# Kernel optimization log

Measured on AMD Instinct MI355X. Metric: run time of the kernel, lower is better.

The kernel has to match this reference:

```python
import jax, jax.numpy as jnp
import numpy as np

N_NODES = 10000
N_EDGES = 80000
F_IN = 128
H1 = 2048
H2 = 2048
H3 = 1024


def _sgconv(x, pos, src, dst, W_in, b_in, W_out, b_out):
    # geo-GCN SpatialGraphConv with hidden_size=1:
    # message(j->i) = relu(Linear(pos_j - pos_i)) * x_j ; aggr='add' ; then Linear out
    rel = pos[src] - pos[dst]                      # [E, 2]  (pos_j - pos_i)
    scale = jax.nn.relu(rel @ W_in + b_in)         # [E, C_in]
    msg = scale * x[src]                           # [E, C_in]
    agg = jax.ops.segment_sum(msg, dst, num_segments=x.shape[0])  # [N, C_in]
    return agg @ W_out + b_out                     # [N, C_out]


def setup_inputs() -> dict:
    key = jax.random.key(0)
    ks = jax.random.split(key, 12)
    x = jax.random.normal(ks[0], (N_NODES, F_IN), dtype=jnp.float32)
    pos = jax.random.normal(ks[1], (N_NODES, 2), dtype=jnp.float32)
    edge_index = jax.random.randint(ks[2], (2, N_EDGES), 0, N_NODES, dtype=jnp.int32)

    def lin(k, fan_in, fan_out):
        lim = 1.0 / np.sqrt(fan_in)
        kw, kb = jax.random.split(k)
        W = jax.random.uniform(kw, (fan_in, fan_out), jnp.float32, -lim, lim)
        b = jax.random.uniform(kb, (fan_out,), jnp.float32, -lim, lim)
        return W, b

    W_in1, b_in1 = lin(ks[3], 2, F_IN)
    W_out1, b_out1 = lin(ks[4], F_IN, H1)
    W_in2, b_in2 = lin(ks[5], 2, H1)
    W_out2, b_out2 = lin(ks[6], H1, H2)
    W_in3, b_in3 = lin(ks[7], 2, H2)
    W_out3, b_out3 = lin(ks[8], H2, H3)

    return {
        "x": x, "pos": pos, "edge_index": edge_index,
        "W_in1": W_in1, "b_in1": b_in1, "W_out1": W_out1, "b_out1": b_out1,
        "W_in2": W_in2, "b_in2": b_in2, "W_out2": W_out2, "b_out2": b_out2,
        "W_in3": W_in3, "b_in3": b_in3, "W_out3": W_out3, "b_out3": b_out3,
    }


def reference(x, pos, edge_index,
              W_in1, b_in1, W_out1, b_out1,
              W_in2, b_in2, W_out2, b_out2,
              W_in3, b_in3, W_out3, b_out3):
    src, dst = edge_index[0], edge_index[1]  # flow source_to_target: j=src, i=dst
    h = jax.nn.relu(_sgconv(x, pos, src, dst, W_in1, b_in1, W_out1, b_out1))
    h = jax.nn.relu(_sgconv(h, pos, src, dst, W_in2, b_in2, W_out2, b_out2))
    h = jax.nn.relu(_sgconv(h, pos, src, dst, W_in3, b_in3, W_out3, b_out3))
    # F.normalize(h, dim=1): L2 normalize rows with eps clamp 1e-12
    norm = jnp.linalg.norm(h, axis=1, keepdims=True)
    return h / jnp.maximum(norm, 1e-12)
```

## Files before the change

### kernel.cpp

```cpp
#include <hip/hip_runtime.h>
#include <hip/hip_bf16.h>

#define DEVI __device__ __forceinline__

constexpr int NN = 10000;
constexpr int NE = 80000;
constexpr int AGG_ROWS = 10240;
constexpr int ES_CAP = 110016;

typedef __attribute__((ext_vector_type(8))) short bf16x8;
typedef __attribute__((ext_vector_type(4))) float f32x4;

DEVI float blo(unsigned int u) {
  union { unsigned int i; float f; } c; c.i = u << 16; return c.f;
}
DEVI float bhi(unsigned int u) {
  union { unsigned int i; float f; } c; c.i = u & 0xffff0000u; return c.f;
}
DEVI unsigned short f2b(float f) {
  union { float f; unsigned int i; } c; c.f = f;
  unsigned int i = c.i;
  return (unsigned short)((i + 0x7fffu + ((i >> 16) & 1u)) >> 16);
}
DEVI void st1(float* p, float v) { *p = v; }
DEVI void st1(unsigned short* p, float v) { *p = f2b(v); }
DEVI void store8b(unsigned short* p, const float v[8]) {
  int4 pk;
  pk.x = (int)((unsigned)f2b(v[0]) | ((unsigned)f2b(v[1]) << 16));
  pk.y = (int)((unsigned)f2b(v[2]) | ((unsigned)f2b(v[3]) << 16));
  pk.z = (int)((unsigned)f2b(v[4]) | ((unsigned)f2b(v[5]) << 16));
  pk.w = (int)((unsigned)f2b(v[6]) | ((unsigned)f2b(v[7]) << 16));
  *reinterpret_cast<int4*>(p) = pk;
}

DEVI void gload16(const void* g, void* l) {
  __builtin_amdgcn_global_load_lds(
      (const __attribute__((address_space(1))) void*)g,
      (__attribute__((address_space(3))) void*)l, 16, 0, 0);
}

__global__ __launch_bounds__(256)
void hist_kernel(const int* __restrict__ dst, int* __restrict__ cnt) {
  int e = blockIdx.x * 256 + threadIdx.x;
  if (e < NE) atomicAdd(&cnt[dst[e]], 1);
}

__global__ __launch_bounds__(1024)
void scan_kernel(const int* __restrict__ cnt, int* __restrict__ off,
                 int* __restrict__ cursor) {
  __shared__ int wpart[16];
  __shared__ int carry;
  int tid = threadIdx.x, lane = tid & 63, w = tid >> 6;
  if (tid == 0) carry = 0;
  __syncthreads();
  for (int base = 0; base < NN; base += 1024) {
    int i = base + tid;
    int v = (i < NN) ? ((cnt[i] + 3) & ~3) : 0;
    int s = v;
#pragma unroll
    for (int o = 1; o < 64; o <<= 1) { int t = __shfl_up(s, o); if (lane >= o) s += t; }
    if (lane == 63) wpart[w] = s;
    __syncthreads();
    if (w == 0) {
      int ws = (lane < 16) ? wpart[lane] : 0;
#pragma unroll
      for (int o = 1; o < 16; o <<= 1) { int t = __shfl_up(ws, o); if (lane >= o) ws += t; }
      if (lane < 16) wpart[lane] = ws;
    }
    __syncthreads();
    int ex = carry + (w ? wpart[w - 1] : 0) + s - v;
    if (i < NN) { off[i] = ex; cursor[i] = ex; }
    __syncthreads();
    if (tid == 0) carry += wpart[15];
    __syncthreads();
  }
}

__global__ __launch_bounds__(256)
void bucket_kernel(const int* __restrict__ src, const int* __restrict__ dst,
                   const float* __restrict__ pos,
                   int* __restrict__ cursor, int* __restrict__ es,
                   float* __restrict__ rel) {
  int e = blockIdx.x * 256 + threadIdx.x;
  if (e < NE) {
    int s = src[e], d = dst[e];
    int p = atomicAdd(&cursor[d], 1);
    float2 ps = *reinterpret_cast<const float2*>(pos + 2 * s);
    float2 pd = *reinterpret_cast<const float2*>(pos + 2 * d);
    es[p] = s;
    *reinterpret_cast<float2*>(rel + 2 * p) = make_float2(ps.x - pd.x, ps.y - pd.y);
  }
}

__global__ __launch_bounds__(256)
void transpose_w(const float* __restrict__ W, unsigned short* __restrict__ WT,
                 int K, int N) {
  __shared__ float tile[32][33];
  int tx = threadIdx.x & 31, ty = threadIdx.x >> 5;
  int n0 = blockIdx.x * 32, k0 = blockIdx.y * 32;
#pragma unroll
  for (int j = 0; j < 32; j += 8)
    tile[ty + j][tx] = W[(size_t)(k0 + ty + j) * N + n0 + tx];
  __syncthreads();
#pragma unroll
  for (int j = 0; j < 32; j += 8)
    WT[(size_t)(n0 + ty + j) * K + k0 + tx] = f2b(tile[tx][ty + j]);
}

__global__ __launch_bounds__(256)
void gather_l1(const float* __restrict__ x,
               const int* __restrict__ off, const int* __restrict__ cnt,
               const int* __restrict__ es, const float* __restrict__ rel,
               const float* __restrict__ Win, const float* __restrict__ bin,
               unsigned short* __restrict__ agg) {
  constexpr int C = 128;
  int lane = threadIdx.x & 63;
  int i = blockIdx.x * 4 + (threadIdx.x >> 6);
  if (i >= NN) return;
  int c = lane * 2;
  float w00 = Win[c], w01 = Win[c + 1];
  float w10 = Win[C + c], w11 = Win[C + c + 1];
  float b0 = bin[c], b1 = bin[c + 1];
  float a0 = 0.f, a1 = 0.f;
  int s0 = off[i], n = cnt[i];

  for (int k = 0; k < n; k += 4) {
    int4 s4 = *reinterpret_cast<const int4*>(es + s0 + k);
    float4 ra = *reinterpret_cast<const float4*>(rel + 2 * (s0 + k));
    float4 rb = *reinterpret_cast<const float4*>(rel + 2 * (s0 + k) + 4);
    float2 q0 = *reinterpret_cast<const float2*>(x + (size_t)s4.x * C + c);
    float2 q1 = *reinterpret_cast<const float2*>(x + (size_t)s4.y * C + c);
    float2 q2 = *reinterpret_cast<const float2*>(x + (size_t)s4.z * C + c);
    float2 q3 = *reinterpret_cast<const float2*>(x + (size_t)s4.w * C + c);
    {
      float sc0 = fmaxf(fmaf(ra.x, w00, fmaf(ra.y, w10, b0)), 0.f);
      float sc1 = fmaxf(fmaf(ra.x, w01, fmaf(ra.y, w11, b1)), 0.f);
      a0 = fmaf(sc0, q0.x, a0); a1 = fmaf(sc1, q0.y, a1);
    }
    if (k + 1 < n) {
      float sc0 = fmaxf(fmaf(ra.z, w00, fmaf(ra.w, w10, b0)), 0.f);
      float sc1 = fmaxf(fmaf(ra.z, w01, fmaf(ra.w, w11, b1)), 0.f);
      a0 = fmaf(sc0, q1.x, a0); a1 = fmaf(sc1, q1.y, a1);
    }
    if (k + 2 < n) {
      float sc0 = fmaxf(fmaf(rb.x, w00, fmaf(rb.y, w10, b0)), 0.f);
      float sc1 = fmaxf(fmaf(rb.x, w01, fmaf(rb.y, w11, b1)), 0.f);
      a0 = fmaf(sc0, q2.x, a0); a1 = fmaf(sc1, q2.y, a1);
    }
    if (k + 3 < n) {
      float sc0 = fmaxf(fmaf(rb.z, w00, fmaf(rb.w, w10, b0)), 0.f);
      float sc1 = fmaxf(fmaf(rb.z, w01, fmaf(rb.w, w11, b1)), 0.f);
      a0 = fmaf(sc0, q3.x, a0); a1 = fmaf(sc1, q3.y, a1);
    }
  }
  unsigned int pk = (unsigned)f2b(a0) | ((unsigned)f2b(a1) << 16);
  *reinterpret_cast<unsigned int*>(agg + (size_t)i * C + c) = pk;
}

__global__ __launch_bounds__(256)
void gather_chunk(const unsigned short* __restrict__ x,
                  const int* __restrict__ off, const int* __restrict__ cnt,
                  const int* __restrict__ es, const float* __restrict__ rel,
                  const float* __restrict__ Win, const float* __restrict__ bin,
                  unsigned short* __restrict__ agg, int ngb8) {
  constexpr int C = 2048;
  constexpr int V = 8;
  int wgid = blockIdx.x;
  int half = wgid >= ngb8;
  int base = half ? wgid - ngb8 : wgid;
  int chunk = (base & 7) + (half << 3);
  int grp = base >> 3;
  int lane = threadIdx.x & 63;
  int wid = threadIdx.x >> 6;
  int slot = lane >> 4;
  int l16 = lane & 15;
  int i = grp * 16 + wid * 4 + slot;
  int c = chunk * 128 + l16 * V;

  float w0[V], w1[V], bb[V], acc[V];
#pragma unroll
  for (int j = 0; j < V; ++j) {
    w0[j] = Win[c + j]; w1[j] = Win[C + c + j]; bb[j] = bin[c + j]; acc[j] = 0.f;
  }
  int s0 = off[i], n = cnt[i];

  auto fma8 = [&](float rx, float ry, const int4& q) {
    float xv[V] = { blo(q.x), bhi(q.x), blo(q.y), bhi(q.y),
                    blo(q.z), bhi(q.z), blo(q.w), bhi(q.w) };
#pragma unroll
    for (int j = 0; j < V; ++j) {
      float sc = fmaxf(fmaf(rx, w0[j], fmaf(ry, w1[j], bb[j])), 0.f);
      acc[j] = fmaf(sc, xv[j], acc[j]);
    }
  };
  for (int k = 0; k < n; k += 4) {
    int4 s4 = *reinterpret_cast<const int4*>(es + s0 + k);
    float4 ra = *reinterpret_cast<const float4*>(rel + 2 * (s0 + k));
    float4 rb = *reinterpret_cast<const float4*>(rel + 2 * (s0 + k) + 4);
    int4 q0 = *reinterpret_cast<const int4*>(x + (size_t)s4.x * C + c);
    int4 q1 = *reinterpret_cast<const int4*>(x + (size_t)s4.y * C + c);
    int4 q2 = *reinterpret_cast<const int4*>(x + (size_t)s4.z * C + c);
    int4 q3 = *reinterpret_cast<const int4*>(x + (size_t)s4.w * C + c);
    fma8(ra.x, ra.y, q0);
    if (k + 1 < n) fma8(ra.z, ra.w, q1);
    if (k + 2 < n) fma8(rb.x, rb.y, q2);
    if (k + 3 < n) fma8(rb.z, rb.w, q3);
  }
  store8b(agg + (size_t)i * C + c, acc);
}

template <typename OT>
__global__ __launch_bounds__(512, 2)
void gemm8p(const unsigned short* __restrict__ A,
            const unsigned short* __restrict__ BT,
            const float* __restrict__ bias, OT* __restrict__ out,
            int M, int N, int K) {
  extern __shared__ unsigned short lds[];
  const int t = threadIdx.x;
  const int lane = t & 63, wid = t >> 6;
  const int wr = wid >> 2, wc = wid & 3;

  const int nwg = gridDim.x * gridDim.y;
  const int orig = blockIdx.y * gridDim.x + blockIdx.x;
  const int swz = (orig & 7) * (nwg >> 3) + (orig >> 3);
  const int bx = swz % gridDim.x, by = swz / gridDim.x;
  const int m0 = by * 320, n0 = bx * 256;
  const int nk = K >> 6;

  const int srow = t >> 3;
  const int schunk = (t & 7) ^ (srow & 7);
  const unsigned short* gA = A + (size_t)(m0 + srow) * K + schunk * 8;
  const unsigned short* gB = BT + (size_t)(n0 + srow) * K + schunk * 8;
  const int lt8 = t * 8;

  auto STAGE = [&](int buf, int kt) {
    const size_t ko = (size_t)kt << 6;
    unsigned short* lb = lds + buf * 36864;
#pragma unroll
    for (int jj = 0; jj < 5; ++jj)
      gload16(gA + (size_t)(jj * 64) * K + ko, lb + jj * 4096 + lt8);
#pragma unroll
    for (int jj = 0; jj < 4; ++jj)
      gload16(gB + (size_t)(jj * 64) * K + ko, lb + 20480 + jj * 4096 + lt8);
  };

  const int frow = lane & 15, kc = lane >> 4;
  const int sl0 = (kc ^ (frow & 7)) * 8;
  const int paRow = (wr * 160 + frow) * 64;
  const int pbRow = 20480 + (wc * 64 + frow) * 64;

  f32x4 acc[10][4];
#pragma unroll
  for (int m = 0; m < 10; ++m)
#pragma unroll
    for (int n = 0; n < 4; ++n) acc[m][n] = 0.f;

  STAGE(0, 0);

  int cur = 0;
  for (int kt = 0; kt < nk; ++kt) {
    if (kt + 1 < nk) {
      STAGE(cur ^ 1, kt + 1);
      asm volatile("s_waitcnt vmcnt(9)" ::: "memory");
    } else {
      asm volatile("s_waitcnt vmcnt(0)" ::: "memory");
    }
    __builtin_amdgcn_s_barrier();
    const unsigned short* pa = lds + cur * 36864 + paRow;
    const unsigned short* pb = lds + cur * 36864 + pbRow;
    bf16x8 bf[4], af[5];

#pragma unroll
    for (int n = 0; n < 4; ++n)
      bf[n] = *reinterpret_cast<const bf16x8*>(pb + n * 1024 + sl0);
#pragma unroll
    for (int m = 0; m < 5; ++m)
      af[m] = *reinterpret_cast<const bf16x8*>(pa + m * 1024 + sl0);
    __builtin_amdgcn_s_barrier();
    __builtin_amdgcn_s_setprio(1);
#pragma unroll
    for (int m = 0; m < 5; ++m)
#pragma unroll
      for (int n = 0; n < 4; ++n)
        acc[m][n] = __builtin_amdgcn_mfma_f32_16x16x32_bf16(
            af[m], bf[n], acc[m][n], 0, 0, 0);
    __builtin_amdgcn_s_setprio(0);
    __builtin_amdgcn_s_barrier();

#pragma unroll
    for (int m = 0; m < 5; ++m)
      af[m] = *reinterpret_cast<const bf16x8*>(pa + (5 + m) * 1024 + sl0);
    __builtin_amdgcn_s_barrier();
    __builtin_amdgcn_s_setprio(1);
#pragma unroll
    for (int m = 0; m < 5; ++m)
#pragma unroll
      for (int n = 0; n < 4; ++n)
        acc[5 + m][n] = __builtin_amdgcn_mfma_f32_16x16x32_bf16(
            af[m], bf[n], acc[5 + m][n], 0, 0, 0);
    __builtin_amdgcn_s_setprio(0);
    __builtin_amdgcn_s_barrier();

#pragma unroll
    for (int n = 0; n < 4; ++n)
      bf[n] = *reinterpret_cast<const bf16x8*>(pb + n * 1024 + (sl0 ^ 32));
#pragma unroll
    for (int m = 0; m < 5; ++m)
      af[m] = *reinterpret_cast<const bf16x8*>(pa + m * 1024 + (sl0 ^ 32));
    __builtin_amdgcn_s_barrier();
    __builtin_amdgcn_s_setprio(1);
#pragma unroll
    for (int m = 0; m < 5; ++m)
#pragma unroll
      for (int n = 0; n < 4; ++n)
        acc[m][n] = __builtin_amdgcn_mfma_f32_16x16x32_bf16(
            af[m], bf[n], acc[m][n], 0, 0, 0);
    __builtin_amdgcn_s_setprio(0);
    __builtin_amdgcn_s_barrier();

#pragma unroll
    for (int m = 0; m < 5; ++m)
      af[m] = *reinterpret_cast<const bf16x8*>(pa + (5 + m) * 1024 + (sl0 ^ 32));
    __builtin_amdgcn_s_barrier();
    __builtin_amdgcn_s_setprio(1);
#pragma unroll
    for (int m = 0; m < 5; ++m)
#pragma unroll
      for (int n = 0; n < 4; ++n)
        acc[5 + m][n] = __builtin_amdgcn_mfma_f32_16x16x32_bf16(
            af[m], bf[n], acc[5 + m][n], 0, 0, 0);
    __builtin_amdgcn_s_setprio(0);
    __builtin_amdgcn_s_barrier();
    cur ^= 1;
  }

  const int ccol = lane & 15;
  const int crow = (lane >> 4) * 4;
  float bv[4];
#pragma unroll
  for (int n = 0; n < 4; ++n)
    bv[n] = bias[n0 + wc * 64 + n * 16 + ccol];
#pragma unroll
  for (int m = 0; m < 10; ++m) {
    int gm0 = m0 + wr * 160 + m * 16 + crow;
#pragma unroll
    for (int r = 0; r < 4; ++r) {
      int gm = gm0 + r;
      if (gm < M) {
        size_t base = (size_t)gm * N + n0 + wc * 64 + ccol;
#pragma unroll
        for (int n = 0; n < 4; ++n)
          st1(out + base + n * 16, fmaxf(acc[m][n][r] + bv[n], 0.f));
      }
    }
  }
}

__global__ __launch_bounds__(256)
void l2norm_kernel(float* __restrict__ out) {
  constexpr int C = 1024;
  float* p = out + (size_t)blockIdx.x * C;
  float4 v = *reinterpret_cast<const float4*>(p + threadIdx.x * 4);
  float s = v.x * v.x + v.y * v.y + v.z * v.z + v.w * v.w;
#pragma unroll
  for (int o = 32; o > 0; o >>= 1) s += __shfl_down(s, o);
  __shared__ float wsum[4];
  if ((threadIdx.x & 63) == 0) wsum[threadIdx.x >> 6] = s;
  __syncthreads();
  float tot = wsum[0] + wsum[1] + wsum[2] + wsum[3];
  float inv = 1.0f / fmaxf(sqrtf(tot), 1e-12f);
  float4 r = make_float4(v.x * inv, v.y * inv, v.z * inv, v.w * inv);
  *reinterpret_cast<float4*>(p + threadIdx.x * 4) = r;
}

extern "C" void kernel_launch(void* const* d_in, const int* in_sizes, int n_in,
                              void* d_out, int out_size, void* d_ws, size_t ws_size,
                              hipStream_t stream) {
  (void)in_sizes; (void)n_in; (void)out_size; (void)ws_size;
  const float* x     = (const float*)d_in[0];
  const float* pos   = (const float*)d_in[1];
  const int*   ei    = (const int*)d_in[2];
  const int*   srcv  = ei;
  const int*   dstv  = ei + NE;
  const float* Win1  = (const float*)d_in[3];
  const float* bin1  = (const float*)d_in[4];
  const float* Wout1 = (const float*)d_in[5];
  const float* bout1 = (const float*)d_in[6];
  const float* Win2  = (const float*)d_in[7];
  const float* bin2  = (const float*)d_in[8];
  const float* Wout2 = (const float*)d_in[9];
  const float* bout2 = (const float*)d_in[10];
  const float* Win3  = (const float*)d_in[11];
  const float* bin3  = (const float*)d_in[12];
  const float* Wout3 = (const float*)d_in[13];
  const float* bout3 = (const float*)d_in[14];
  float* outp = (float*)d_out;

  char* ws = (char*)d_ws;
  unsigned short* aggb = (unsigned short*)ws;
  unsigned short* h1   = (unsigned short*)(ws + 41943040);
  unsigned short* W2T  = (unsigned short*)(ws + 82903040);
  unsigned short* W3T  = (unsigned short*)(ws + 91291648);
  unsigned short* W1T  = (unsigned short*)(ws + 95485952);
  int* cnt    = (int*)(ws + 96010240);
  int* off    = (int*)(ws + 96050240);
  int* cursor = (int*)(ws + 96090240);
  int* es     = (int*)(ws + 96130240);
  float* rel  = (float*)(ws + 96570304);
  unsigned short* h2 = (unsigned short*)d_out;

  hipFuncSetAttribute((const void*)gemm8p<unsigned short>,
                      hipFuncAttributeMaxDynamicSharedMemorySize, 147456);
  hipFuncSetAttribute((const void*)gemm8p<float>,
                      hipFuncAttributeMaxDynamicSharedMemorySize, 147456);

  const dim3 blk(256);
  const int eb = (NE + 255) / 256;
  const int ngb8 = ((NN + 15) / 16) * 8;

  hipMemsetAsync(cnt, 0, NN * sizeof(int), stream);
  hipMemsetAsync(es, 0, ES_CAP * sizeof(int), stream);
  hist_kernel<<<eb, blk, 0, stream>>>(dstv, cnt);
  scan_kernel<<<1, 1024, 0, stream>>>(cnt, off, cursor);
  bucket_kernel<<<eb, blk, 0, stream>>>(srcv, dstv, pos, cursor, es, rel);

  transpose_w<<<dim3(2048 / 32, 128 / 32),  blk, 0, stream>>>(Wout1, W1T, 128, 2048);
  transpose_w<<<dim3(2048 / 32, 2048 / 32), blk, 0, stream>>>(Wout2, W2T, 2048, 2048);
  transpose_w<<<dim3(1024 / 32, 2048 / 32), blk, 0, stream>>>(Wout3, W3T, 2048, 1024);

  hipMemsetAsync(aggb + (size_t)NN * 2048, 0, (size_t)(AGG_ROWS - NN) * 2048 * 2, stream);

  gather_l1<<<(NN + 3) / 4, blk, 0, stream>>>(x, off, cnt, es, rel, Win1, bin1, aggb);
  gemm8p<unsigned short><<<dim3(2048 / 256, AGG_ROWS / 320), 512, 147456, stream>>>(
      aggb, W1T, bout1, h1, NN, 2048, 128);

  gather_chunk<<<2 * ngb8, blk, 0, stream>>>(h1, off, cnt, es, rel, Win2, bin2, aggb, ngb8);
  gemm8p<unsigned short><<<dim3(2048 / 256, AGG_ROWS / 320), 512, 147456, stream>>>(
      aggb, W2T, bout2, h2, NN, 2048, 2048);

  gather_chunk<<<2 * ngb8, blk, 0, stream>>>(h2, off, cnt, es, rel, Win3, bin3, aggb, ngb8);
  gemm8p<float><<<dim3(1024 / 256, AGG_ROWS / 320), 512, 147456, stream>>>(
      aggb, W3T, bout3, outp, NN, 1024, 2048);

  l2norm_kernel<<<NN, blk, 0, stream>>>(outp);
}
```

Baseline: 342.5 us.

## Interleave GEMM prefetch with MFMA phases, add smaller-tile GEMM for layer 3, merge transposes

The main GEMM now issues the next K-tile's global-to-LDS loads in small groups spread across the four MFMA phases, instead of all at once before the barrier. The goal is to overlap memory traffic with compute and reduce the wait at each iteration. Layer 3 (N=1024) switches to a new 160x128-tile, 256-thread kernel that launches more workgroups, which should fill the CUs better. The three weight transposes are merged into one launch. The risks are a different waitcnt schedule and fewer barriers in the new kernel, which could cause races or worse MFMA utilisation.

```diff
diff --git a/kernel.cpp b/kernel.cpp
--- a/kernel.cpp
+++ b/kernel.cpp
@@ -93,11 +93,20 @@
 }
 
 __global__ __launch_bounds__(256)
-void transpose_w(const float* __restrict__ W, unsigned short* __restrict__ WT,
-                 int K, int N) {
+void transpose_w3(const float* __restrict__ W1, unsigned short* __restrict__ T1,
+                  const float* __restrict__ W2, unsigned short* __restrict__ T2,
+                  const float* __restrict__ W3, unsigned short* __restrict__ T3) {
   __shared__ float tile[32][33];
+  int b = blockIdx.x;
+  const float* W; unsigned short* WT; int K, N, bx, by;
+  if (b < 256)        { W = W1; WT = T1; K = 128;  N = 2048; b -= 0;
+                        bx = b & 63;  by = b >> 6; }
+  else if (b < 4352)  { W = W2; WT = T2; K = 2048; N = 2048; b -= 256;
+                        bx = b & 63;  by = b >> 6; }
+  else                { W = W3; WT = T3; K = 2048; N = 1024; b -= 4352;
+                        bx = b & 31;  by = b >> 5; }
   int tx = threadIdx.x & 31, ty = threadIdx.x >> 5;
-  int n0 = blockIdx.x * 32, k0 = blockIdx.y * 32;
+  int n0 = bx * 32, k0 = by * 32;
 #pragma unroll
   for (int j = 0; j < 32; j += 8)
     tile[ty + j][tx] = W[(size_t)(k0 + ty + j) * N + n0 + tx];
@@ -211,7 +220,7 @@
 
 template <typename OT>
 __global__ __launch_bounds__(512, 2)
-void gemm8p(const unsigned short* __restrict__ A,
+void gemm4p(const unsigned short* __restrict__ A,
             const unsigned short* __restrict__ BT,
             const float* __restrict__ bias, OT* __restrict__ out,
             int M, int N, int K) {
@@ -233,15 +242,14 @@
   const unsigned short* gB = BT + (size_t)(n0 + srow) * K + schunk * 8;
   const int lt8 = t * 8;
 
-  auto STAGE = [&](int buf, int kt) {
+  auto PASS = [&](int buf, int kt, int j) {
     const size_t ko = (size_t)kt << 6;
     unsigned short* lb = lds + buf * 36864;
-#pragma unroll
-    for (int jj = 0; jj < 5; ++jj)
-      gload16(gA + (size_t)(jj * 64) * K + ko, lb + jj * 4096 + lt8);
-#pragma unroll
-    for (int jj = 0; jj < 4; ++jj)
-      gload16(gB + (size_t)(jj * 64) * K + ko, lb + 20480 + jj * 4096 + lt8);
+    if (j < 5)
+      gload16(gA + (size_t)(j * 64) * K + ko, lb + j * 4096 + lt8);
+    else
+      gload16(gB + (size_t)((j - 5) * 64) * K + ko,
+              lb + 20480 + (j - 5) * 4096 + lt8);
   };
 
   const int frow = lane & 15, kc = lane >> 4;
@@ -252,6 +260,161 @@
   f32x4 acc[10][4];
 #pragma unroll
   for (int m = 0; m < 10; ++m)
+#pragma unroll
+    for (int n = 0; n < 4; ++n) acc[m][n] = 0.f;
+
+#pragma unroll
+  for (int j = 0; j < 9; ++j) PASS(0, 0, j);
+
+  int cur = 0;
+  for (int kt = 0; kt < nk; ++kt) {
+    const bool pf = (kt + 1 < nk);
+    const unsigned short* pa = lds + cur * 36864 + paRow;
+    const unsigned short* pb = lds + cur * 36864 + pbRow;
+    bf16x8 bf[4], af[5];
+
+    if (pf) {
+      PASS(cur ^ 1, kt + 1, 0); PASS(cur ^ 1, kt + 1, 1);
+      asm volatile("s_waitcnt vmcnt(2)" ::: "memory");
+    } else {
+      asm volatile("s_waitcnt vmcnt(0)" ::: "memory");
+    }
+    __builtin_amdgcn_s_barrier();
+#pragma unroll
+    for (int n = 0; n < 4; ++n)
+      bf[n] = *reinterpret_cast<const bf16x8*>(pb + n * 1024 + sl0);
+#pragma unroll
+    for (int m = 0; m < 5; ++m)
+      af[m] = *reinterpret_cast<const bf16x8*>(pa + m * 1024 + sl0);
+    __builtin_amdgcn_s_barrier();
+    __builtin_amdgcn_s_setprio(1);
+#pragma unroll
+    for (int m = 0; m < 5; ++m)
+#pragma unroll
+      for (int n = 0; n < 4; ++n)
+        acc[m][n] = __builtin_amdgcn_mfma_f32_16x16x32_bf16(
+            af[m], bf[n], acc[m][n], 0, 0, 0);
+    __builtin_amdgcn_s_setprio(0);
+    __builtin_amdgcn_s_barrier();
+
+    if (pf) { PASS(cur ^ 1, kt + 1, 2); PASS(cur ^ 1, kt + 1, 3); }
+#pragma unroll
+    for (int m = 0; m < 5; ++m)
+      af[m] = *reinterpret_cast<const bf16x8*>(pa + (5 + m) * 1024 + sl0);
+    __builtin_amdgcn_s_barrier();
+    __builtin_amdgcn_s_setprio(1);
+#pragma unroll
+    for (int m = 0; m < 5; ++m)
+#pragma unroll
+      for (int n = 0; n < 4; ++n)
+        acc[5 + m][n] = __builtin_amdgcn_mfma_f32_16x16x32_bf16(
+            af[m], bf[n], acc[5 + m][n], 0, 0, 0);
+    __builtin_amdgcn_s_setprio(0);
+    __builtin_amdgcn_s_barrier();
+
+    if (pf) { PASS(cur ^ 1, kt + 1, 4); PASS(cur ^ 1, kt + 1, 5); }
+#pragma unroll
+    for (int n = 0; n < 4; ++n)
+      bf[n] = *reinterpret_cast<const bf16x8*>(pb + n * 1024 + (sl0 ^ 32));
+#pragma unroll
+    for (int m = 0; m < 5; ++m)
+      af[m] = *reinterpret_cast<const bf16x8*>(pa + m * 1024 + (sl0 ^ 32));
+    __builtin_amdgcn_s_barrier();
+    __builtin_amdgcn_s_setprio(1);
+#pragma unroll
+    for (int m = 0; m < 5; ++m)
+#pragma unroll
+      for (int n = 0; n < 4; ++n)
+        acc[m][n] = __builtin_amdgcn_mfma_f32_16x16x32_bf16(
+            af[m], bf[n], acc[m][n], 0, 0, 0);
+    __builtin_amdgcn_s_setprio(0);
+    __builtin_amdgcn_s_barrier();
+
+    if (pf) { PASS(cur ^ 1, kt + 1, 6); PASS(cur ^ 1, kt + 1, 7);
+              PASS(cur ^ 1, kt + 1, 8); }
+#pragma unroll
+    for (int m = 0; m < 5; ++m)
+      af[m] = *reinterpret_cast<const bf16x8*>(pa + (5 + m) * 1024 + (sl0 ^ 32));
+    __builtin_amdgcn_s_barrier();
+    __builtin_amdgcn_s_setprio(1);
+#pragma unroll
+    for (int m = 0; m < 5; ++m)
+#pragma unroll
+      for (int n = 0; n < 4; ++n)
+        acc[5 + m][n] = __builtin_amdgcn_mfma_f32_16x16x32_bf16(
+            af[m], bf[n], acc[5 + m][n], 0, 0, 0);
+    __builtin_amdgcn_s_setprio(0);
+    __builtin_amdgcn_s_barrier();
+    cur ^= 1;
+  }
+
+  const int ccol = lane & 15;
+  const int crow = (lane >> 4) * 4;
+  float bv[4];
+#pragma unroll
+  for (int n = 0; n < 4; ++n)
+    bv[n] = bias[n0 + wc * 64 + n * 16 + ccol];
+#pragma unroll
+  for (int m = 0; m < 10; ++m) {
+    int gm0 = m0 + wr * 160 + m * 16 + crow;
+#pragma unroll
+    for (int r = 0; r < 4; ++r) {
+      int gm = gm0 + r;
+      if (gm < M) {
+        size_t base = (size_t)gm * N + n0 + wc * 64 + ccol;
+#pragma unroll
+        for (int n = 0; n < 4; ++n)
+          st1(out + base + n * 16, fmaxf(acc[m][n][r] + bv[n], 0.f));
+      }
+    }
+  }
+}
+
+template <typename OT>
+__global__ __launch_bounds__(256, 2)
+void gemm160(const unsigned short* __restrict__ A,
+             const unsigned short* __restrict__ BT,
+             const float* __restrict__ bias, OT* __restrict__ out,
+             int M, int N, int K) {
+  extern __shared__ unsigned short lds[];
+  const int t = threadIdx.x;
+  const int lane = t & 63, wid = t >> 6;
+  const int wr = wid >> 1, wc = wid & 1;
+
+  const int nwg = gridDim.x * gridDim.y;
+  const int orig = blockIdx.y * gridDim.x + blockIdx.x;
+  const int swz = (orig & 7) * (nwg >> 3) + (orig >> 3);
+  const int bx = swz % gridDim.x, by = swz / gridDim.x;
+  const int m0 = by * 160, n0 = bx * 128;
+  const int nk = K >> 6;
+
+  const int lrow = lane >> 3;
+  const int schunk = (lane & 7) ^ lrow;
+  const unsigned short* gA = A + (size_t)(m0 + wid * 40 + lrow) * K + schunk * 8;
+  const unsigned short* gB = BT + (size_t)(n0 + wid * 32 + lrow) * K + schunk * 8;
+  unsigned short* lA = lds + (wid * 5) * 512 + lane * 8;
+  unsigned short* lB = lds + 20480 + (wid * 4) * 512 + lane * 8;
+
+  auto STAGE = [&](int buf, int kt) {
+    const size_t ko = (size_t)kt << 6;
+#pragma unroll
+    for (int jj = 0; jj < 5; ++jj)
+      gload16(gA + (size_t)(jj * 8) * K + ko, lA + buf * 10240 + jj * 512);
+#pragma unroll
+    for (int jj = 0; jj < 4; ++jj)
+      gload16(gB + (size_t)(jj * 8) * K + ko, lB + buf * 8192 + jj * 512);
+  };
+
+  const int frow = lane & 15;
+  const int fr7 = frow & 7;
+  const int slot0 = ((lane >> 4) ^ fr7) * 8;
+  const int slot1 = ((4 + (lane >> 4)) ^ fr7) * 8;
+  const int paRow = (wr * 80 + frow) * 64;
+  const int pbRow = (wc * 64 + frow) * 64;
+
+  f32x4 acc[5][4];
+#pragma unroll
+  for (int m = 0; m < 5; ++m)
 #pragma unroll
     for (int n = 0; n < 4; ++n) acc[m][n] = 0.f;
 
@@ -265,72 +428,29 @@
     } else {
       asm volatile("s_waitcnt vmcnt(0)" ::: "memory");
     }
-    __builtin_amdgcn_s_barrier();
-    const unsigned short* pa = lds + cur * 36864 + paRow;
-    const unsigned short* pb = lds + cur * 36864 + pbRow;
-    bf16x8 bf[4], af[5];
-
-#pragma unroll
-    for (int n = 0; n < 4; ++n)
-      bf[n] = *reinterpret_cast<const bf16x8*>(pb + n * 1024 + sl0);
-#pragma unroll
-    for (int m = 0; m < 5; ++m)
-      af[m] = *reinterpret_cast<const bf16x8*>(pa + m * 1024 + sl0);
-    __builtin_amdgcn_s_barrier();
-    __builtin_amdgcn_s_setprio(1);
-#pragma unroll
-    for (int m = 0; m < 5; ++m)
+    asm volatile("s_barrier" ::: "memory");
+    const unsigned short* pa = lds + cur * 10240 + paRow;
+    const unsigned short* pb = lds + 20480 + cur * 8192 + pbRow;
+#pragma unroll
+    for (int ks = 0; ks < 2; ++ks) {
+      const int sl = ks ? slot1 : slot0;
+      bf16x8 af[5], bf[4];
+#pragma unroll
+      for (int m = 0; m < 5; ++m)
+        af[m] = *reinterpret_cast<const bf16x8*>(pa + m * 1024 + sl);
 #pragma unroll
       for (int n = 0; n < 4; ++n)
-        acc[m][n] = __builtin_amdgcn_mfma_f32_16x16x32_bf16(
-            af[m], bf[n], acc[m][n], 0, 0, 0);
-    __builtin_amdgcn_s_setprio(0);
-    __builtin_amdgcn_s_barrier();
-
-#pragma unroll
-    for (int m = 0; m < 5; ++m)
-      af[m] = *reinterpret_cast<const bf16x8*>(pa + (5 + m) * 1024 + sl0);
-    __builtin_amdgcn_s_barrier();
-    __builtin_amdgcn_s_setprio(1);
-#pragma unroll
-    for (int m = 0; m < 5; ++m)
-#pragma unroll
-      for (int n = 0; n < 4; ++n)
-        acc[5 + m][n] = __builtin_amdgcn_mfma_f32_16x16x32_bf16(
-            af[m], bf[n], acc[5 + m][n], 0, 0, 0);
-    __builtin_amdgcn_s_setprio(0);
-    __builtin_amdgcn_s_barrier();
-
-#pragma unroll
-    for (int n = 0; n < 4; ++n)
-      bf[n] = *reinterpret_cast<const bf16x8*>(pb + n * 1024 + (sl0 ^ 32));
-#pragma unroll
-    for (int m = 0; m < 5; ++m)
-      af[m] = *reinterpret_cast<const bf16x8*>(pa + m * 1024 + (sl0 ^ 32));
-    __builtin_amdgcn_s_barrier();
-    __builtin_amdgcn_s_setprio(1);
-#pragma unroll
-    for (int m = 0; m < 5; ++m)
-#pragma unroll
-      for (int n = 0; n < 4; ++n)
-        acc[m][n] = __builtin_amdgcn_mfma_f32_16x16x32_bf16(
-            af[m], bf[n], acc[m][n], 0, 0, 0);
-    __builtin_amdgcn_s_setprio(0);
-    __builtin_amdgcn_s_barrier();
-
-#pragma unroll
-    for (int m = 0; m < 5; ++m)
-      af[m] = *reinterpret_cast<const bf16x8*>(pa + (5 + m) * 1024 + (sl0 ^ 32));
-    __builtin_amdgcn_s_barrier();
-    __builtin_amdgcn_s_setprio(1);
-#pragma unroll
-    for (int m = 0; m < 5; ++m)
-#pragma unroll
-      for (int n = 0; n < 4; ++n)
-        acc[5 + m][n] = __builtin_amdgcn_mfma_f32_16x16x32_bf16(
-            af[m], bf[n], acc[5 + m][n], 0, 0, 0);
-    __builtin_amdgcn_s_setprio(0);
-    __builtin_amdgcn_s_barrier();
+        bf[n] = *reinterpret_cast<const bf16x8*>(pb + n * 1024 + sl);
+      __builtin_amdgcn_s_setprio(1);
+#pragma unroll
+      for (int m = 0; m < 5; ++m)
+#pragma unroll
+        for (int n = 0; n < 4; ++n)
+          acc[m][n] = __builtin_amdgcn_mfma_f32_16x16x32_bf16(
+              af[m], bf[n], acc[m][n], 0, 0, 0);
+      __builtin_amdgcn_s_setprio(0);
+    }
+    asm volatile("s_barrier" ::: "memory");
     cur ^= 1;
   }
 
@@ -341,8 +461,8 @@
   for (int n = 0; n < 4; ++n)
     bv[n] = bias[n0 + wc * 64 + n * 16 + ccol];
 #pragma unroll
-  for (int m = 0; m < 10; ++m) {
-    int gm0 = m0 + wr * 160 + m * 16 + crow;
+  for (int m = 0; m < 5; ++m) {
+    int gm0 = m0 + wr * 80 + m * 16 + crow;
 #pragma unroll
     for (int r = 0; r < 4; ++r) {
       int gm = gm0 + r;
@@ -409,10 +529,10 @@
   float* rel  = (float*)(ws + 96570304);
   unsigned short* h2 = (unsigned short*)d_out;
 
-  hipFuncSetAttribute((const void*)gemm8p<unsigned short>,
+  hipFuncSetAttribute((const void*)gemm4p<unsigned short>,
                       hipFuncAttributeMaxDynamicSharedMemorySize, 147456);
-  hipFuncSetAttribute((const void*)gemm8p<float>,
-                      hipFuncAttributeMaxDynamicSharedMemorySize, 147456);
+  hipFuncSetAttribute((const void*)gemm160<float>,
+                      hipFuncAttributeMaxDynamicSharedMemorySize, 73728);
 
   const dim3 blk(256);
   const int eb = (NE + 255) / 256;
@@ -424,22 +544,20 @@
   scan_kernel<<<1, 1024, 0, stream>>>(cnt, off, cursor);
   bucket_kernel<<<eb, blk, 0, stream>>>(srcv, dstv, pos, cursor, es, rel);
 
-  transpose_w<<<dim3(2048 / 32, 128 / 32),  blk, 0, stream>>>(Wout1, W1T, 128, 2048);
-  transpose_w<<<dim3(2048 / 32, 2048 / 32), blk, 0, stream>>>(Wout2, W2T, 2048, 2048);
-  transpose_w<<<dim3(1024 / 32, 2048 / 32), blk, 0, stream>>>(Wout3, W3T, 2048, 1024);
+  transpose_w3<<<6400, blk, 0, stream>>>(Wout1, W1T, Wout2, W2T, Wout3, W3T);
 
   hipMemsetAsync(aggb + (size_t)NN * 2048, 0, (size_t)(AGG_ROWS - NN) * 2048 * 2, stream);
 
   gather_l1<<<(NN + 3) / 4, blk, 0, stream>>>(x, off, cnt, es, rel, Win1, bin1, aggb);
-  gemm8p<unsigned short><<<dim3(2048 / 256, AGG_ROWS / 320), 512, 147456, stream>>>(
+  gemm4p<unsigned short><<<dim3(2048 / 256, AGG_ROWS / 320), 512, 147456, stream>>>(
       aggb, W1T, bout1, h1, NN, 2048, 128);
 
   gather_chunk<<<2 * ngb8, blk, 0, stream>>>(h1, off, cnt, es, rel, Win2, bin2, aggb, ngb8);
-  gemm8p<unsigned short><<<dim3(2048 / 256, AGG_ROWS / 320), 512, 147456, stream>>>(
+  gemm4p<unsigned short><<<dim3(2048 / 256, AGG_ROWS / 320), 512, 147456, stream>>>(
       aggb, W2T, bout2, h2, NN, 2048, 2048);
 
   gather_chunk<<<2 * ngb8, blk, 0, stream>>>(h2, off, cnt, es, rel, Win3, bin3, aggb, ngb8);
-  gemm8p<float><<<dim3(1024 / 256, AGG_ROWS / 320), 512, 147456, stream>>>(
+  gemm160<float><<<dim3(1024 / 128, AGG_ROWS / 160), blk, 73728, stream>>>(
       aggb, W3T, bout3, outp, NN, 1024, 2048);
 
   l2norm_kernel<<<NN, blk, 0, stream>>>(outp);
```

Result: faster. 300.6 us (-12.2%).
